# Optimization experiments

Measured on AMD Instinct MI355X. Metric: run time of the kernel, lower is better.

## Reference

```python
import jax, jax.numpy as jnp
import numpy as np

N = 50000      # num nodes
E = 800000     # num edges
F_IN = 100     # input features (ogbn-products)
HID = 128      # hidden_dim (per-head out_channels)
H = 2          # heads
OUT = 47       # num classes
NEG_SLOPE = 0.2


def setup_inputs() -> dict:
    key = jax.random.key(0)
    ks = jax.random.split(key, 14)
    def glorot(k, shape, fan):
        return jax.random.normal(k, shape, jnp.float32) * (1.0 / np.sqrt(fan))
    x = jax.random.normal(ks[0], (N, F_IN), jnp.float32)
    edge_index = jax.random.randint(ks[1], (2, E), 0, N)
    # GAT layer 0: lin_l (= lin_r, shared) weight [H*HID, F_IN], attention vecs [H, HID]
    W0 = glorot(ks[2], (H * HID, F_IN), F_IN)
    b0 = jnp.zeros((H * HID,), jnp.float32)
    attl0 = glorot(ks[3], (H, HID), HID)
    attr0 = glorot(ks[4], (H, HID), HID)
    # GAT layer 1: input dim H*HID
    W1 = glorot(ks[5], (H * HID, H * HID), H * HID)
    b1 = jnp.zeros((H * HID,), jnp.float32)
    attl1 = glorot(ks[6], (H, HID), HID)
    attr1 = glorot(ks[7], (H, HID), HID)
    # post_mp: Linear(H*HID -> HID), Linear(HID -> OUT)
    Wp1 = glorot(ks[8], (HID, H * HID), H * HID)
    bp1 = jnp.zeros((HID,), jnp.float32)
    Wp2 = glorot(ks[9], (OUT, HID), HID)
    bp2 = jnp.zeros((OUT,), jnp.float32)
    return dict(x=x, edge_index=edge_index, W0=W0, b0=b0, attl0=attl0, attr0=attr0,
                W1=W1, b1=b1, attl1=attl1, attr1=attr1,
                Wp1=Wp1, bp1=bp1, Wp2=Wp2, bp2=bp2)


def gat_layer(x, W, b, att_l, att_r, src, dst):
    # shared lin_l == lin_r in the source
    h = (x @ W.T + b).reshape(-1, H, HID)          # [N, H, C]
    alpha_l = jnp.einsum('nhc,hc->nh', h, att_l)   # per-node left scores
    alpha_r = jnp.einsum('nhc,hc->nh', h, att_r)   # per-node right scores
    e = jax.nn.leaky_relu(alpha_l[src] + alpha_r[dst], NEG_SLOPE)  # [E, H]
    # segment softmax over edges grouped by destination node
    emax = jax.ops.segment_max(e, dst, num_segments=N)             # [N, H]
    ee = jnp.exp(e - emax[dst])
    denom = jax.ops.segment_sum(ee, dst, num_segments=N)           # [N, H]
    a = ee / denom[dst]                                            # [E, H]
    msg = a[:, :, None] * h[src]                                   # [E, H, C]
    out = jax.ops.segment_sum(msg, dst, num_segments=N)            # [N, H, C]
    return out.reshape(-1, H * HID)


def reference(x, edge_index, W0, b0, attl0, attr0, W1, b1, attl1, attr1, Wp1, bp1, Wp2, bp2):
    src, dst = edge_index[0], edge_index[1]
    x = jax.nn.relu(gat_layer(x, W0, b0, attl0, attr0, src, dst))
    x = jax.nn.relu(gat_layer(x, W1, b1, attl1, attr1, src, dst))
    h = x @ Wp1.T + bp1           # dropout p=0.0 -> identity
    logits = h @ Wp2.T + bp2
    return jax.nn.log_softmax(logits, axis=1)
```

## Files before the change

kernel.cpp:

```cpp
#include <hip/hip_runtime.h>
#include <math.h>

#define N_NODES 50000
#define E_EDGES 800000
#define F_IN 100
#define HID 128
#define HEADS 2
#define OUT_C 47
#define HH (HEADS*HID)
#define MPAD 50048
#define NB_GEMM 782
#define NB_AUX  910

typedef float floatx4 __attribute__((ext_vector_type(4)));
typedef short short8 __attribute__((ext_vector_type(8)));

__device__ inline ushort bf16round(float v) {
    unsigned u = __float_as_uint(v);
    return (ushort)((u + 0x7FFFu + ((u >> 16) & 1u)) >> 16);
}

__device__ __forceinline__ void gl_lds16(const void* g, void* l) {
    __builtin_amdgcn_global_load_lds(
        (const __attribute__((address_space(1))) unsigned int*)g,
        (__attribute__((address_space(3))) unsigned int*)l, 16, 0, 0);
}

template<bool F32IN>
__device__ __forceinline__ void gemm_body(
    int bx, int by,
    const ushort* __restrict__ Ab, const float* __restrict__ Axf,
    const ushort* __restrict__ Wb, const float* __restrict__ Wxf,
    const float* __restrict__ bias,
    ushort* __restrict__ Hb,
    const float* __restrict__ attl, const float* __restrict__ attr,
    float* __restrict__ al, float* __restrict__ ar,
    int M, int Kp, ushort* sA, ushort* sB)
{
    const int t = threadIdx.x;
    const int wave = t >> 6, lane = t & 63;
    const int quad = lane >> 4, l16 = lane & 15;
    const int rl = lane >> 2, seg = lane & 3;
    const int m0 = by * 128, n0 = bx * 128;

    floatx4 acc[2][8];
#pragma unroll
    for (int i = 0; i < 2; i++)
#pragma unroll
        for (int j = 0; j < 8; j++) acc[i][j] = (floatx4)(0.f);

    for (int k0 = 0; k0 < Kp; k0 += 32) {
        if (F32IN) {
#pragma unroll
            for (int i = 0; i < 2; i++) {
                int idx = t + i * 256;
                int row = idx >> 2, sg = idx & 3;
                int gm = m0 + row;
                float f[8];
#pragma unroll
                for (int j = 0; j < 2; j++) {
                    int kb = k0 + sg * 8 + j * 4;
                    float4 v = (gm < M && kb < F_IN)
                        ? *(const float4*)(Axf + (size_t)gm * F_IN + kb)
                        : make_float4(0.f, 0.f, 0.f, 0.f);
                    f[j*4+0] = v.x; f[j*4+1] = v.y; f[j*4+2] = v.z; f[j*4+3] = v.w;
                }
                ushort hh[8];
#pragma unroll
                for (int j = 0; j < 8; j++) hh[j] = bf16round(f[j]);
                *(uint4*)(sA + row * 32 + sg * 8) = *(uint4*)hh;
            }
#pragma unroll
            for (int i = 0; i < 2; i++) {
                int idx = t + i * 256;
                int row = idx >> 2, sg = idx & 3;
                int gn = n0 + row;
                float f[8];
#pragma unroll
                for (int j = 0; j < 2; j++) {
                    int kb = k0 + sg * 8 + j * 4;
                    float4 v = (kb < F_IN)
                        ? *(const float4*)(Wxf + (size_t)gn * F_IN + kb)
                        : make_float4(0.f, 0.f, 0.f, 0.f);
                    f[j*4+0] = v.x; f[j*4+1] = v.y; f[j*4+2] = v.z; f[j*4+3] = v.w;
                }
                ushort hh[8];
#pragma unroll
                for (int j = 0; j < 8; j++) hh[j] = bf16round(f[j]);
                *(uint4*)(sB + row * 32 + sg * 8) = *(uint4*)hh;
            }
        } else {
#pragma unroll
            for (int j = 0; j < 2; j++) {
                int br = wave * 32 + j * 16;
                size_t gro = (size_t)(m0 + br + rl) * Kp + k0 + seg * 8;
                gl_lds16(Ab + gro, sA + br * 32);
            }
#pragma unroll
            for (int j = 0; j < 2; j++) {
                int br = wave * 32 + j * 16;
                size_t gro = (size_t)(n0 + br + rl) * Kp + k0 + seg * 8;
                gl_lds16(Wb + gro, sB + br * 32);
            }
        }
        __syncthreads();

        short8 af[2];
#pragma unroll
        for (int sm = 0; sm < 2; sm++) {
            int r = wave * 32 + sm * 16 + l16;
            af[sm] = *(const short8*)(sA + r * 32 + quad * 8);
        }
#pragma unroll
        for (int sn = 0; sn < 8; sn++) {
            int r = sn * 16 + l16;
            short8 b = *(const short8*)(sB + r * 32 + quad * 8);
#pragma unroll
            for (int sm = 0; sm < 2; sm++)
                acc[sm][sn] = __builtin_amdgcn_mfma_f32_16x16x32_bf16(af[sm], b, acc[sm][sn], 0, 0, 0);
        }
        __syncthreads();
    }

    float bias_r[8], att_l[8], att_r[8];
#pragma unroll
    for (int sn = 0; sn < 8; sn++) {
        int ai = n0 + sn * 16 + l16;
        bias_r[sn] = bias[ai];
        att_l[sn] = attl[ai];
        att_r[sn] = attr[ai];
    }
#pragma unroll
    for (int sm = 0; sm < 2; sm++)
#pragma unroll
        for (int r = 0; r < 4; r++) {
            int gm = m0 + wave * 32 + sm * 16 + quad * 4 + r;
            float suml = 0.f, sumr = 0.f;
#pragma unroll
            for (int sn = 0; sn < 8; sn++) {
                float v = acc[sm][sn][r] + bias_r[sn];
                suml += v * att_l[sn];
                sumr += v * att_r[sn];
                if (gm < M) {
                    int gn = n0 + sn * 16 + l16;
                    Hb[(size_t)gm * 256 + gn] = bf16round(v);
                }
            }
#pragma unroll
            for (int off = 1; off < 16; off <<= 1) {
                suml += __shfl_xor(suml, off);
                sumr += __shfl_xor(sumr, off);
            }
            if (l16 == 0 && gm < M) {
                al[gm * HEADS + bx] = suml;
                ar[gm * HEADS + bx] = sumr;
            }
        }
}

__global__ __launch_bounds__(256) void k_l0_count(
    const float* __restrict__ x, const float* __restrict__ W0,
    const float* __restrict__ b0,
    const float* __restrict__ attl0, const float* __restrict__ attr0,
    ushort* __restrict__ hb, float* __restrict__ al, float* __restrict__ ar,
    const int* __restrict__ dstv, int* __restrict__ deg, ushort* __restrict__ rank,
    const float* __restrict__ W1, const float* __restrict__ Wp1,
    const float* __restrict__ Wp2,
    ushort* __restrict__ W1b, ushort* __restrict__ Wp1b, ushort* __restrict__ Wp2b)
{
    __shared__ ushort sA[128 * 32], sB[128 * 32];
    const int b = blockIdx.x;
    if (b < NB_GEMM) {
        gemm_body<true>(b & 1, b >> 1, nullptr, x, nullptr, W0, b0,
                        hb, attl0, attr0, al, ar, N_NODES, 128, sA, sB);
    } else {
        const int c1 = HH * HH;
        const int c2 = c1 + HID * HH;
        const int c3 = c2 + 64 * HID;
        int base = (b - NB_GEMM) * 256 + threadIdx.x;
        for (int i = base; i < E_EDGES + c3; i += NB_AUX * 256) {
            if (i < E_EDGES) {
                int d = dstv[i];
                int r = atomicAdd(&deg[d], 1);
                rank[i] = (ushort)r;
            } else {
                int j = i - E_EDGES;
                float v; ushort* H; int jj;
                if (j < c1)      { jj = j;      v = W1[jj];  H = W1b; }
                else if (j < c2) { jj = j - c1; v = Wp1[jj]; H = Wp1b; }
                else {
                    jj = j - c2;
                    int r2 = jj >> 7;
                    v = (r2 < OUT_C) ? Wp2[jj] : 0.f;
                    H = Wp2b;
                }
                H[jj] = bf16round(v);
            }
        }
    }
}

__global__ void scan_local(const int* __restrict__ cnt, int* __restrict__ excl,
                           int* __restrict__ bsum, int Nn) {
    __shared__ int s[256];
    int t = threadIdx.x;
    int i = blockIdx.x * 256 + t;
    int v = (i < Nn) ? cnt[i] : 0;
    s[t] = v;
    __syncthreads();
    for (int off = 1; off < 256; off <<= 1) {
        int add = (t >= off) ? s[t - off] : 0;
        __syncthreads();
        s[t] += add;
        __syncthreads();
    }
    int incl = s[t];
    if (i < Nn) excl[i] = incl - v;
    if (t == 255) bsum[blockIdx.x] = incl;
}

__global__ void scan_bsum(int* bsum, int nblk) {
    __shared__ int s[256];
    int t = threadIdx.x;
    int v = (t < nblk) ? bsum[t] : 0;
    s[t] = v;
    __syncthreads();
    for (int off = 1; off < 256; off <<= 1) {
        int add = (t >= off) ? s[t - off] : 0;
        __syncthreads();
        s[t] += add;
        __syncthreads();
    }
    int incl = s[t];
    if (t < nblk) bsum[t] = incl - v;
}

__global__ void scan_add(int* __restrict__ rowptr, const int* __restrict__ bsum,
                         int Nn, int Etot) {
    int i = blockIdx.x * 256 + threadIdx.x;
    if (i < Nn) rowptr[i] += bsum[blockIdx.x];
    if (i == 0) rowptr[Nn] = Etot;
}

__global__ void fill_csr16(const int* __restrict__ src, const int* __restrict__ dst,
                           const int* __restrict__ rowptr, const ushort* __restrict__ rank,
                           ushort* __restrict__ csr16, int E) {
    int e = blockIdx.x * 256 + threadIdx.x;
    if (e < E) {
        int pos = rowptr[dst[e]] + (int)rank[e];
        csr16[pos] = (ushort)src[e];
    }
}

__global__ __launch_bounds__(256) void gat_aggregate(
    const ushort* __restrict__ hb, const float* __restrict__ al, const float* __restrict__ ar,
    const int* __restrict__ rowptr, const ushort* __restrict__ csr16,
    ushort* __restrict__ outb)
{
    const int node = blockIdx.x * 4 + (threadIdx.x >> 6);
    const int lane = threadIdx.x & 63;
    if (node >= N_NODES) return;
    const int beg = rowptr[node], end = rowptr[node + 1];
    const int half = lane >> 5;
    const int l32  = lane & 31;
    const int headf = l32 >> 4;
    const float2 ard = ((const float2*)ar)[node];

    float dsum0 = 0.f, dsum1 = 0.f;
    float a[8];
#pragma unroll
    for (int j = 0; j < 8; j++) a[j] = 0.f;

    for (int c0 = beg; c0 < end; c0 += 64) {
        const int n = min(64, end - c0);
        int s = 0; float w0 = 0.f, w1 = 0.f;
        if (lane < n) {
            s = (int)csr16[c0 + lane];
            float2 aa = ((const float2*)al)[s];
            float e0 = aa.x + ard.x;
            float e1 = aa.y + ard.y;
            e0 = fmaxf(e0, 0.f) + 0.2f * fminf(e0, 0.f);
            e1 = fmaxf(e1, 0.f) + 0.2f * fminf(e1, 0.f);
            w0 = __expf(e0); w1 = __expf(e1);
            dsum0 += w0; dsum1 += w1;
        }
        for (int i = 0; i < n; i += 4) {
            int e0i = i + half;
            int   se0 = __shfl(s,  e0i);
            float u00 = __shfl(w0, e0i);
            float u01 = __shfl(w1, e0i);
            float we0 = headf ? u01 : u00;
            const uint4 q0 = *(const uint4*)(hb + (size_t)se0 * 256 + l32 * 8);
            int e1i = i + 2 + half;
            int   se1 = __shfl(s,  e1i);
            float u10 = __shfl(w0, e1i);
            float u11 = __shfl(w1, e1i);
            float we1 = headf ? u11 : u10;
            const uint4 q1 = *(const uint4*)(hb + (size_t)se1 * 256 + l32 * 8);
            a[0] += we0 * __uint_as_float(q0.x << 16);
            a[1] += we0 * __uint_as_float(q0.x & 0xFFFF0000u);
            a[2] += we0 * __uint_as_float(q0.y << 16);
            a[3] += we0 * __uint_as_float(q0.y & 0xFFFF0000u);
            a[4] += we0 * __uint_as_float(q0.z << 16);
            a[5] += we0 * __uint_as_float(q0.z & 0xFFFF0000u);
            a[6] += we0 * __uint_as_float(q0.w << 16);
            a[7] += we0 * __uint_as_float(q0.w & 0xFFFF0000u);
            a[0] += we1 * __uint_as_float(q1.x << 16);
            a[1] += we1 * __uint_as_float(q1.x & 0xFFFF0000u);
            a[2] += we1 * __uint_as_float(q1.y << 16);
            a[3] += we1 * __uint_as_float(q1.y & 0xFFFF0000u);
            a[4] += we1 * __uint_as_float(q1.z << 16);
            a[5] += we1 * __uint_as_float(q1.z & 0xFFFF0000u);
            a[6] += we1 * __uint_as_float(q1.w << 16);
            a[7] += we1 * __uint_as_float(q1.w & 0xFFFF0000u);
        }
    }
#pragma unroll
    for (int j = 0; j < 8; j++) a[j] += __shfl_xor(a[j], 32);
#pragma unroll
    for (int off = 32; off; off >>= 1) {
        dsum0 += __shfl_xor(dsum0, off);
        dsum1 += __shfl_xor(dsum1, off);
    }
    if (half == 0) {
        const float den = headf ? dsum1 : dsum0;
        const float inv = (end > beg) ? 1.f / den : 0.f;
        ushort r[8];
#pragma unroll
        for (int j = 0; j < 8; j++) r[j] = bf16round(fmaxf(a[j] * inv, 0.f));
        *(uint4*)(outb + (size_t)node * 256 + l32 * 8) = *(uint4*)r;
    }
}

__global__ __launch_bounds__(256) void gemm_l1(
    const ushort* __restrict__ Ab, const ushort* __restrict__ Wb,
    const float* __restrict__ bias, ushort* __restrict__ Hb,
    const float* __restrict__ attl, const float* __restrict__ attr,
    float* __restrict__ al, float* __restrict__ ar)
{
    __shared__ ushort sA[128 * 32], sB[128 * 32];
    gemm_body<false>(blockIdx.x, blockIdx.y, Ab, nullptr, Wb, nullptr, bias,
                     Hb, attl, attr, al, ar, N_NODES, HH, sA, sB);
}

__global__ __launch_bounds__(256) void fused_post(
    const ushort* __restrict__ Ab,
    const ushort* __restrict__ Bb,
    const float* __restrict__ bp1,
    const ushort* __restrict__ W2b,
    const float* __restrict__ bp2,
    float* __restrict__ out, int M)
{
    __shared__ ushort sA[128 * 32];
    __shared__ ushort sB[128 * 32];
    __shared__ ushort sP[128 * 136];

    const int t = threadIdx.x;
    const int wave = t >> 6, lane = t & 63;
    const int quad = lane >> 4, l16 = lane & 15;
    const int rl = lane >> 2, seg = lane & 3;
    const int m0 = blockIdx.x * 128;

    floatx4 acc[2][8];
#pragma unroll
    for (int i = 0; i < 2; i++)
#pragma unroll
        for (int j = 0; j < 8; j++) acc[i][j] = (floatx4)(0.f);

    for (int k0 = 0; k0 < HH; k0 += 32) {
#pragma unroll
        for (int j = 0; j < 2; j++) {
            int br = wave * 32 + j * 16;
            size_t gro = (size_t)(m0 + br + rl) * HH + k0 + seg * 8;
            gl_lds16(Ab + gro, sA + br * 32);
        }
#pragma unroll
        for (int j = 0; j < 2; j++) {
            int br = wave * 32 + j * 16;
            size_t gro = (size_t)(br + rl) * HH + k0 + seg * 8;
            gl_lds16(Bb + gro, sB + br * 32);
        }
        __syncthreads();
        short8 af[2];
#pragma unroll
        for (int sm = 0; sm < 2; sm++) {
            int r = wave * 32 + sm * 16 + l16;
            af[sm] = *(const short8*)(sA + r * 32 + quad * 8);
        }
#pragma unroll
        for (int sn = 0; sn < 8; sn++) {
            int r = sn * 16 + l16;
            short8 b = *(const short8*)(sB + r * 32 + quad * 8);
#pragma unroll
            for (int sm = 0; sm < 2; sm++)
                acc[sm][sn] = __builtin_amdgcn_mfma_f32_16x16x32_bf16(af[sm], b, acc[sm][sn], 0, 0, 0);
        }
        __syncthreads();
    }
#pragma unroll
    for (int sm = 0; sm < 2; sm++)
#pragma unroll
        for (int sn = 0; sn < 8; sn++)
#pragma unroll
            for (int r = 0; r < 4; r++) {
                int row = wave * 32 + sm * 16 + quad * 4 + r;
                int col = sn * 16 + l16;
                sP[row * 136 + col] = bf16round(acc[sm][sn][r] + bp1[col]);
            }
    __syncthreads();

    floatx4 acc2[2][4];
#pragma unroll
    for (int i = 0; i < 2; i++)
#pragma unroll
        for (int j = 0; j < 4; j++) acc2[i][j] = (floatx4)(0.f);

    for (int k0 = 0; k0 < HID; k0 += 32) {
        {
            int br = wave * 16;
            size_t gro = (size_t)(br + rl) * HID + k0 + seg * 8;
            gl_lds16(W2b + gro, sA + br * 32);
        }
        __syncthreads();
        short8 ph[2];
#pragma unroll
        for (int sm = 0; sm < 2; sm++) {
            int r = wave * 32 + sm * 16 + l16;
            ph[sm] = *(const short8*)(sP + r * 136 + k0 + quad * 8);
        }
#pragma unroll
        for (int sn = 0; sn < 4; sn++) {
            int r = sn * 16 + l16;
            short8 b = *(const short8*)(sA + r * 32 + quad * 8);
#pragma unroll
            for (int sm = 0; sm < 2; sm++)
                acc2[sm][sn] = __builtin_amdgcn_mfma_f32_16x16x32_bf16(ph[sm], b, acc2[sm][sn], 0, 0, 0);
        }
        __syncthreads();
    }

    float b2[4];
#pragma unroll
    for (int sn = 0; sn < 4; sn++) {
        int n = sn * 16 + l16;
        b2[sn] = (n < OUT_C) ? bp2[n] : 0.f;
    }
#pragma unroll
    for (int sm = 0; sm < 2; sm++)
#pragma unroll
        for (int r = 0; r < 4; r++) {
            float v[4];
            float m = -INFINITY;
#pragma unroll
            for (int sn = 0; sn < 4; sn++) {
                int n = sn * 16 + l16;
                float xv = (n < OUT_C) ? acc2[sm][sn][r] + b2[sn] : -INFINITY;
                v[sn] = xv;
                m = fmaxf(m, xv);
            }
#pragma unroll
            for (int off = 1; off < 16; off <<= 1) m = fmaxf(m, __shfl_xor(m, off));
            float ssum = 0.f;
#pragma unroll
            for (int sn = 0; sn < 4; sn++) {
                int n = sn * 16 + l16;
                if (n < OUT_C) ssum += __expf(v[sn] - m);
            }
#pragma unroll
            for (int off = 1; off < 16; off <<= 1) ssum += __shfl_xor(ssum, off);
            float lse = m + logf(ssum);
            int gm = m0 + wave * 32 + sm * 16 + quad * 4 + r;
            if (gm < M) {
#pragma unroll
                for (int sn = 0; sn < 4; sn++) {
                    int n = sn * 16 + l16;
                    if (n < OUT_C) out[(size_t)gm * OUT_C + n] = v[sn] - lse;
                }
            }
        }
}

extern "C" void kernel_launch(void* const* d_in, const int* in_sizes, int n_in,
                              void* d_out, int out_size, void* d_ws, size_t ws_size,
                              hipStream_t stream) {
    const float* x     = (const float*)d_in[0];
    const int*   ei    = (const int*)d_in[1];
    const float* W0    = (const float*)d_in[2];
    const float* b0    = (const float*)d_in[3];
    const float* attl0 = (const float*)d_in[4];
    const float* attr0 = (const float*)d_in[5];
    const float* W1    = (const float*)d_in[6];
    const float* b1    = (const float*)d_in[7];
    const float* attl1 = (const float*)d_in[8];
    const float* attr1 = (const float*)d_in[9];
    const float* Wp1   = (const float*)d_in[10];
    const float* bp1   = (const float*)d_in[11];
    const float* Wp2   = (const float*)d_in[12];
    const float* bp2   = (const float*)d_in[13];
    float* out = (float*)d_out;

    const int Nn = N_NODES, Etot = E_EDGES;
    const int* srcv = ei;
    const int* dstv = ei + Etot;

    char* ws = (char*)d_ws;
    size_t off = 0;
    auto alloc = [&](size_t bytes) -> void* {
        void* p = ws + off;
        off = (off + bytes + 255) & ~(size_t)255;
        return p;
    };
    int*    rowptr = (int*)alloc((size_t)(Nn + 1) * sizeof(int));
    int*    deg    = (int*)alloc((size_t)Nn * sizeof(int));
    ushort* rank   = (ushort*)alloc((size_t)Etot * 2);
    ushort* csr16  = (ushort*)alloc((size_t)Etot * 2);
    int*    bsum   = (int*)alloc(256 * sizeof(int));
    float*  al     = (float*)alloc((size_t)Nn * HEADS * sizeof(float));
    float*  ar     = (float*)alloc((size_t)Nn * HEADS * sizeof(float));
    ushort* W1b    = (ushort*)alloc((size_t)HH * HH * 2);
    ushort* Wp1b   = (ushort*)alloc((size_t)HID * HH * 2);
    ushort* Wp2b   = (ushort*)alloc((size_t)64 * HID * 2);
    ushort* hb     = (ushort*)alloc((size_t)Nn * HH * 2);
    ushort* xbb    = (ushort*)alloc((size_t)MPAD * HH * 2);

    const int nblk = (Nn + 255) / 256;

    hipMemsetAsync(deg, 0, (size_t)Nn * sizeof(int), stream);

    k_l0_count<<<NB_GEMM + NB_AUX, 256, 0, stream>>>(
        x, W0, b0, attl0, attr0, hb, al, ar,
        dstv, deg, rank, W1, Wp1, Wp2, W1b, Wp1b, Wp2b);

    scan_local<<<nblk, 256, 0, stream>>>(deg, rowptr, bsum, Nn);
    scan_bsum<<<1, 256, 0, stream>>>(bsum, nblk);
    scan_add<<<nblk, 256, 0, stream>>>(rowptr, bsum, Nn, Etot);
    fill_csr16<<<(Etot + 255) / 256, 256, 0, stream>>>(srcv, dstv, rowptr, rank, csr16, Etot);

    gat_aggregate<<<(Nn + 3) / 4, 256, 0, stream>>>(hb, al, ar, rowptr, csr16, xbb);

    {
        dim3 g(2, MPAD / 128);
        gemm_l1<<<g, 256, 0, stream>>>(xbb, W1b, b1, hb, attl1, attr1, al, ar);
    }
    gat_aggregate<<<(Nn + 3) / 4, 256, 0, stream>>>(hb, al, ar, rowptr, csr16, xbb);

    fused_post<<<MPAD / 128, 256, 0, stream>>>(xbb, Wp1b, bp1, Wp2b, bp2, out, Nn);
}
```

Baseline: 324.2 us.

## Split fused layer-0 GEMM/count kernel and vectorize aggregate accumulators as float2

Breaks the combined kernel, which ran the layer-0 GEMM blocks alongside degree counting and weight conversion, into two launches. One is a flat one-thread-per-element count/convert kernel and the other a dedicated 2D-grid GEMM. It also rewrites the aggregation inner loop to accumulate in float2 vectors so the compiler can emit packed FMA instructions. The split costs one extra launch and removes the overlap between the GEMM and the atomic counting.

```diff
diff --git a/kernel.cpp b/kernel.cpp
--- a/kernel.cpp
+++ b/kernel.cpp
@@ -9,10 +9,9 @@
 #define OUT_C 47
 #define HH (HEADS*HID)
 #define MPAD 50048
-#define NB_GEMM 782
-#define NB_AUX  910
 
 typedef float floatx4 __attribute__((ext_vector_type(4)));
+typedef float float2v __attribute__((ext_vector_type(2)));
 typedef short short8 __attribute__((ext_vector_type(8)));
 
 __device__ inline ushort bf16round(float v) {
@@ -158,45 +157,42 @@
         }
 }
 
-__global__ __launch_bounds__(256) void k_l0_count(
+__global__ __launch_bounds__(256) void gemm_l0(
     const float* __restrict__ x, const float* __restrict__ W0,
     const float* __restrict__ b0,
     const float* __restrict__ attl0, const float* __restrict__ attr0,
-    ushort* __restrict__ hb, float* __restrict__ al, float* __restrict__ ar,
-    const int* __restrict__ dstv, int* __restrict__ deg, ushort* __restrict__ rank,
-    const float* __restrict__ W1, const float* __restrict__ Wp1,
-    const float* __restrict__ Wp2,
-    ushort* __restrict__ W1b, ushort* __restrict__ Wp1b, ushort* __restrict__ Wp2b)
+    ushort* __restrict__ hb, float* __restrict__ al, float* __restrict__ ar)
 {
     __shared__ ushort sA[128 * 32], sB[128 * 32];
-    const int b = blockIdx.x;
-    if (b < NB_GEMM) {
-        gemm_body<true>(b & 1, b >> 1, nullptr, x, nullptr, W0, b0,
-                        hb, attl0, attr0, al, ar, N_NODES, 128, sA, sB);
-    } else {
-        const int c1 = HH * HH;
-        const int c2 = c1 + HID * HH;
-        const int c3 = c2 + 64 * HID;
-        int base = (b - NB_GEMM) * 256 + threadIdx.x;
-        for (int i = base; i < E_EDGES + c3; i += NB_AUX * 256) {
-            if (i < E_EDGES) {
-                int d = dstv[i];
-                int r = atomicAdd(&deg[d], 1);
-                rank[i] = (ushort)r;
-            } else {
-                int j = i - E_EDGES;
-                float v; ushort* H; int jj;
-                if (j < c1)      { jj = j;      v = W1[jj];  H = W1b; }
-                else if (j < c2) { jj = j - c1; v = Wp1[jj]; H = Wp1b; }
-                else {
-                    jj = j - c2;
-                    int r2 = jj >> 7;
-                    v = (r2 < OUT_C) ? Wp2[jj] : 0.f;
-                    H = Wp2b;
-                }
-                H[jj] = bf16round(v);
-            }
-        }
+    gemm_body<true>(blockIdx.x, blockIdx.y, nullptr, x, nullptr, W0, b0,
+                    hb, attl0, attr0, al, ar, N_NODES, 128, sA, sB);
+}
+
+__global__ void count_convert(const int* __restrict__ dstv, int* __restrict__ deg,
+                              ushort* __restrict__ rank,
+                              const float* __restrict__ W1, const float* __restrict__ Wp1,
+                              const float* __restrict__ Wp2,
+                              ushort* __restrict__ W1b, ushort* __restrict__ Wp1b,
+                              ushort* __restrict__ Wp2b) {
+    const int c1 = HH * HH;
+    const int c2 = c1 + HID * HH;
+    const int c3 = c2 + 64 * HID;
+    int i = blockIdx.x * 256 + threadIdx.x;
+    if (i < E_EDGES) {
+        int d = dstv[i];
+        rank[i] = (ushort)atomicAdd(&deg[d], 1);
+    }
+    if (i < c3) {
+        float v; ushort* H; int jj;
+        if (i < c1)      { jj = i;      v = W1[jj];  H = W1b; }
+        else if (i < c2) { jj = i - c1; v = Wp1[jj]; H = Wp1b; }
+        else {
+            jj = i - c2;
+            int r2 = jj >> 7;
+            v = (r2 < OUT_C) ? Wp2[jj] : 0.f;
+            H = Wp2b;
+        }
+        H[jj] = bf16round(v);
     }
 }
 
@@ -267,9 +263,9 @@
     const float2 ard = ((const float2*)ar)[node];
 
     float dsum0 = 0.f, dsum1 = 0.f;
-    float a[8];
-#pragma unroll
-    for (int j = 0; j < 8; j++) a[j] = 0.f;
+    float2v av[4];
+#pragma unroll
+    for (int j = 0; j < 4; j++) av[j] = (float2v)(0.f);
 
     for (int c0 = beg; c0 < end; c0 += 64) {
         const int n = min(64, end - c0);
@@ -289,34 +285,38 @@
             int   se0 = __shfl(s,  e0i);
             float u00 = __shfl(w0, e0i);
             float u01 = __shfl(w1, e0i);
-            float we0 = headf ? u01 : u00;
+            float2v we0 = (float2v)(headf ? u01 : u00);
             const uint4 q0 = *(const uint4*)(hb + (size_t)se0 * 256 + l32 * 8);
             int e1i = i + 2 + half;
             int   se1 = __shfl(s,  e1i);
             float u10 = __shfl(w0, e1i);
             float u11 = __shfl(w1, e1i);
-            float we1 = headf ? u11 : u10;
+            float2v we1 = (float2v)(headf ? u11 : u10);
             const uint4 q1 = *(const uint4*)(hb + (size_t)se1 * 256 + l32 * 8);
-            a[0] += we0 * __uint_as_float(q0.x << 16);
-            a[1] += we0 * __uint_as_float(q0.x & 0xFFFF0000u);
-            a[2] += we0 * __uint_as_float(q0.y << 16);
-            a[3] += we0 * __uint_as_float(q0.y & 0xFFFF0000u);
-            a[4] += we0 * __uint_as_float(q0.z << 16);
-            a[5] += we0 * __uint_as_float(q0.z & 0xFFFF0000u);
-            a[6] += we0 * __uint_as_float(q0.w << 16);
-            a[7] += we0 * __uint_as_float(q0.w & 0xFFFF0000u);
-            a[0] += we1 * __uint_as_float(q1.x << 16);
-            a[1] += we1 * __uint_as_float(q1.x & 0xFFFF0000u);
-            a[2] += we1 * __uint_as_float(q1.y << 16);
-            a[3] += we1 * __uint_as_float(q1.y & 0xFFFF0000u);
-            a[4] += we1 * __uint_as_float(q1.z << 16);
-            a[5] += we1 * __uint_as_float(q1.z & 0xFFFF0000u);
-            a[6] += we1 * __uint_as_float(q1.w << 16);
-            a[7] += we1 * __uint_as_float(q1.w & 0xFFFF0000u);
-        }
-    }
-#pragma unroll
-    for (int j = 0; j < 8; j++) a[j] += __shfl_xor(a[j], 32);
+            float2v p;
+            p.x = __uint_as_float(q0.x << 16); p.y = __uint_as_float(q0.x & 0xFFFF0000u);
+            av[0] += we0 * p;
+            p.x = __uint_as_float(q0.y << 16); p.y = __uint_as_float(q0.y & 0xFFFF0000u);
+            av[1] += we0 * p;
+            p.x = __uint_as_float(q0.z << 16); p.y = __uint_as_float(q0.z & 0xFFFF0000u);
+            av[2] += we0 * p;
+            p.x = __uint_as_float(q0.w << 16); p.y = __uint_as_float(q0.w & 0xFFFF0000u);
+            av[3] += we0 * p;
+            p.x = __uint_as_float(q1.x << 16); p.y = __uint_as_float(q1.x & 0xFFFF0000u);
+            av[0] += we1 * p;
+            p.x = __uint_as_float(q1.y << 16); p.y = __uint_as_float(q1.y & 0xFFFF0000u);
+            av[1] += we1 * p;
+            p.x = __uint_as_float(q1.z << 16); p.y = __uint_as_float(q1.z & 0xFFFF0000u);
+            av[2] += we1 * p;
+            p.x = __uint_as_float(q1.w << 16); p.y = __uint_as_float(q1.w & 0xFFFF0000u);
+            av[3] += we1 * p;
+        }
+    }
+#pragma unroll
+    for (int j = 0; j < 4; j++) {
+        av[j].x += __shfl_xor(av[j].x, 32);
+        av[j].y += __shfl_xor(av[j].y, 32);
+    }
 #pragma unroll
     for (int off = 32; off; off >>= 1) {
         dsum0 += __shfl_xor(dsum0, off);
@@ -327,7 +327,10 @@
         const float inv = (end > beg) ? 1.f / den : 0.f;
         ushort r[8];
 #pragma unroll
-        for (int j = 0; j < 8; j++) r[j] = bf16round(fmaxf(a[j] * inv, 0.f));
+        for (int j = 0; j < 4; j++) {
+            r[2*j]   = bf16round(fmaxf(av[j].x * inv, 0.f));
+            r[2*j+1] = bf16round(fmaxf(av[j].y * inv, 0.f));
+        }
         *(uint4*)(outb + (size_t)node * 256 + l32 * 8) = *(uint4*)r;
     }
 }
@@ -527,9 +530,13 @@
 
     hipMemsetAsync(deg, 0, (size_t)Nn * sizeof(int), stream);
 
-    k_l0_count<<<NB_GEMM + NB_AUX, 256, 0, stream>>>(
-        x, W0, b0, attl0, attr0, hb, al, ar,
+    count_convert<<<(Etot + 255) / 256, 256, 0, stream>>>(
         dstv, deg, rank, W1, Wp1, Wp2, W1b, Wp1b, Wp2b);
+
+    {
+        dim3 g(2, MPAD / 128);
+        gemm_l0<<<g, 256, 0, stream>>>(x, W0, b0, attl0, attr0, hb, al, ar);
+    }
 
     scan_local<<<nblk, 256, 0, stream>>>(deg, rowptr, bsum, Nn);
     scan_bsum<<<1, 256, 0, stream>>>(bsum, nblk);
```

Result: no change. 320.6 us (-1.1%).
